# Performance work log

Measured on AMD Instinct MI355X. Metric: run time of the kernel, lower is better.

## Reference

```python
import jax, jax.numpy as jnp
import numpy as np
from jax import lax

B, C, H, W = 2, 256, 128, 128
NC, NP = 80, 9  # num_classes, num_points (3x3 dcn kernel)
PAD = 1


def conv2d(x, w, b=None, pad=1):
    out = lax.conv_general_dilated(x, w, (1, 1), [(pad, pad), (pad, pad)],
                                   dimension_numbers=('NCHW', 'OIHW', 'NCHW'))
    if b is not None:
        out = out + b[None, :, None, None]
    return out


def bilinear_sample(img_bhwc, py, px):
    # zero-padded bilinear sampling; py/px: [B,H,W] float coords
    Hi, Wi = img_bhwc.shape[1], img_bhwc.shape[2]
    y0 = jnp.floor(py)
    x0 = jnp.floor(px)
    wy1 = py - y0
    wx1 = px - x0

    def gather(yc, xc, w):
        valid = (yc >= 0) & (yc <= Hi - 1) & (xc >= 0) & (xc <= Wi - 1)
        yi = jnp.clip(yc, 0, Hi - 1).astype(jnp.int32)
        xi = jnp.clip(xc, 0, Wi - 1).astype(jnp.int32)
        v = jax.vmap(lambda im, yy, xx: im[yy, xx])(img_bhwc, yi, xi)  # [B,H,W,C]
        return v * (w * valid)[..., None]

    return (gather(y0, x0, (1 - wy1) * (1 - wx1)) + gather(y0, x0 + 1, (1 - wy1) * wx1)
            + gather(y0 + 1, x0, wy1 * (1 - wx1)) + gather(y0 + 1, x0 + 1, wy1 * wx1))


def deform_conv(x, offset, weight, mask=None, pad=1):
    # x: [B,C,H,W]; offset: [B,2K,H,W] interleaved (dy,dx) per kernel point;
    # mask: [B,K,H,W] or None (modulated DCN multiplies sampled value by mask as-is)
    kh, kw = weight.shape[2], weight.shape[3]
    xb = jnp.transpose(x, (0, 2, 3, 1))  # [B,H,W,C]
    gy, gx = jnp.meshgrid(jnp.arange(x.shape[2], dtype=x.dtype),
                          jnp.arange(x.shape[3], dtype=x.dtype), indexing='ij')
    acc = 0.
    for k in range(kh * kw):  # fixed structural loop over 9 kernel points
        ky, kx = k // kw, k % kw
        py = gy[None] + (ky - pad) + offset[:, 2 * k]
        px = gx[None] + (kx - pad) + offset[:, 2 * k + 1]
        val = bilinear_sample(xb, py, px)  # [B,H,W,C]
        if mask is not None:
            val = val * mask[:, k][..., None]
        acc = acc + jnp.einsum('bhwc,oc->bohw', val, weight[:, :, ky, kx])
    return acc


def setup_inputs() -> dict:
    key = jax.random.key(0)
    ks = jax.random.split(key, 16)
    d = {"x": jax.random.normal(ks[0], (B, C, H, W), jnp.float32)}

    def w(k, shape):
        return jax.random.normal(k, shape, jnp.float32) * 0.01

    i = 1
    for j in range(3):
        d[f"cls_w{j}"] = w(ks[i], (C, C, 3, 3)); i += 1
        d[f"cls_b{j}"] = jnp.zeros((C,), jnp.float32)
        d[f"reg_w{j}"] = w(ks[i], (C, C, 3, 3)); i += 1
        d[f"reg_b{j}"] = jnp.zeros((C,), jnp.float32)
    d["init_conv_w"] = w(ks[i], (C, C, 3, 3)); i += 1
    d["init_conv_b"] = jnp.zeros((C,), jnp.float32)
    d["init_out_w"] = w(ks[i], (3 * NP, C, 1, 1)); i += 1
    d["init_out_b"] = jnp.zeros((3 * NP,), jnp.float32)
    d["dcn_cls_w"] = w(ks[i], (C, C, 3, 3)); i += 1  # ModulatedDeformConv (bias=False)
    d["cls_out_w"] = w(ks[i], (NC, C, 1, 1)); i += 1
    d["cls_out_b"] = jnp.full((NC,), -4.59511985013459, jnp.float32)  # bias_init_with_prob(0.01)
    d["dcn_ref_w"] = w(ks[i], (C, C, 3, 3)); i += 1  # DeformConv (bias=False)
    d["ref_out_w"] = w(ks[i], (2 * NP, C, 1, 1)); i += 1
    d["ref_out_b"] = jnp.zeros((2 * NP,), jnp.float32)
    return d


def reference(x, cls_w0, cls_b0, reg_w0, reg_b0, cls_w1, cls_b1, reg_w1, reg_b1,
              cls_w2, cls_b2, reg_w2, reg_b2, init_conv_w, init_conv_b,
              init_out_w, init_out_b, dcn_cls_w, cls_out_w, cls_out_b,
              dcn_ref_w, ref_out_w, ref_out_b):
    relu = jax.nn.relu
    cls_feat = x
    for wgt, b in ((cls_w0, cls_b0), (cls_w1, cls_b1), (cls_w2, cls_b2)):
        cls_feat = relu(conv2d(cls_feat, wgt, b, 1))
    pts_feat = x
    for wgt, b in ((reg_w0, reg_b0), (reg_w1, reg_b1), (reg_w2, reg_b2)):
        pts_feat = relu(conv2d(pts_feat, wgt, b, 1))

    pts_out_init = conv2d(relu(conv2d(pts_feat, init_conv_w, init_conv_b, 1)),
                          init_out_w, init_out_b, 0)  # [B,27,H,W]
    o1, o2, mask = (pts_out_init[:, :NP], pts_out_init[:, NP:2 * NP],
                    pts_out_init[:, 2 * NP:])
    offset = jnp.concatenate([o1, o2], axis=1)  # dcn_offset (points_init = 0)

    cls_out = conv2d(relu(deform_conv(cls_feat, offset, dcn_cls_w, mask)),
                     cls_out_w, cls_out_b, 0)
    pts_out_refine = conv2d(relu(deform_conv(pts_feat, offset, dcn_ref_w)),
                            ref_out_w, ref_out_b, 0)
    pts_out_refine = pts_out_refine + lax.stop_gradient(offset)

    # pts2wh_offsets
    pts = pts_out_refine.reshape(B, NP, 2, H, W)
    pts_mean = pts.mean(axis=1, keepdims=True)          # [B,1,2,H,W]
    wh = jnp.abs(pts + pts_mean).max(axis=1)            # [B,2,H,W]
    reg = pts_mean[:, 0]                                # [B,2,H,W]
    return (cls_out, wh, reg)
```

## Files before the change

kernel.cpp:

```cpp
#include <hip/hip_runtime.h>

#define Bn 2
#define Cn 256
#define Hn 128
#define Wn 128
#define HWn 16384
#define NCn 80

typedef __attribute__((ext_vector_type(4))) float f32x4;
typedef __attribute__((ext_vector_type(8))) short bf16x8;

__device__ __forceinline__ float blo(unsigned u) {
    union { unsigned u; float f; } x; x.u = u << 16; return x.f;
}
__device__ __forceinline__ float bhi(unsigned u) {
    union { unsigned u; float f; } x; x.u = u & 0xffff0000u; return x.f;
}
__device__ __forceinline__ unsigned short f2bf(float f) {
    union { float f; unsigned u; } x; x.f = f;
    unsigned u = x.u + 0x7fffu + ((x.u >> 16) & 1u);
    return (unsigned short)(u >> 16);
}

#define GLOAD16(gp, lp) __builtin_amdgcn_global_load_lds( \
    (__attribute__((address_space(1))) unsigned int*)(gp), \
    (__attribute__((address_space(3))) unsigned int*)(lp), 16, 0, 0)

__global__ void zeroK(unsigned short* z) { z[threadIdx.x] = 0; }

__global__ __launch_bounds__(256) void xinK(const float* __restrict__ x,
                                            unsigned short* __restrict__ o) {
    __shared__ float tb[32][33];
    const int b = blockIdx.z;
    const int hw0 = blockIdx.x * 32, c0 = blockIdx.y * 32;
    const int tx = threadIdx.x & 31, ty = threadIdx.x >> 5;
    const float* ip = x + ((size_t)(b * Cn + c0)) * HWn + hw0;
#pragma unroll
    for (int r = 0; r < 4; ++r) tb[ty + 8 * r][tx] = ip[(size_t)(ty + 8 * r) * HWn + tx];
    __syncthreads();
    unsigned short* op = o + ((size_t)(b * HWn + hw0)) * Cn + c0;
#pragma unroll
    for (int r = 0; r < 4; ++r) op[(size_t)(ty + 8 * r) * Cn + tx] = f2bf(tb[tx][ty + 8 * r]);
}

struct WPtrs { const float* p[9]; };
__global__ __launch_bounds__(256) void repackAll(WPtrs wsrc, unsigned short* __restrict__ dst) {
    const int t = blockIdx.x * 256 + threadIdx.x;
    const int widx = t >> 16;
    const int r = t & 65535;
    const float* s = wsrc.p[widx] + (size_t)r * 9;
    float v[9];
#pragma unroll
    for (int k = 0; k < 9; ++k) v[k] = s[k];
    unsigned short* d = dst + (size_t)widx * 589824 + r;
#pragma unroll
    for (int k = 0; k < 9; ++k) d[(size_t)k * 65536] = f2bf(v[k]);
}

struct HPtrs { const float* w[3]; };
__global__ __launch_bounds__(256) void repackHeads(HPtrs hs, unsigned short* __restrict__ dst) {
    const int t = blockIdx.x * 256 + threadIdx.x;
    const int ic = t & 255, row = t >> 8;
    int which, oc, OC;
    if (row < 32)       { which = 0; oc = row;       OC = 27; }
    else if (row < 128) { which = 1; oc = row - 32;  OC = 80; }
    else                { which = 2; oc = row - 128; OC = 18; }
    dst[t] = (oc < OC) ? f2bf(hs.w[which][(size_t)oc * Cn + ic]) : (unsigned short)0;
}

struct CJobs {
    const unsigned short* feat[2];
    const unsigned short* W[2];
    const float* bias[2];
    unsigned short* out[2];
};
__global__ __launch_bounds__(512, 2) void convGemm256(CJobs jobs,
                                                      const unsigned short* __restrict__ zb) {
    const int jz = blockIdx.z;
    const unsigned short* feat = jobs.feat[jz];
    const unsigned short* Wp = jobs.W[jz];
    const float* bias = jobs.bias[jz];
    unsigned short* outp = jobs.out[jz];

    __shared__ __align__(16) unsigned short lA[2][16384];
    __shared__ __align__(16) unsigned short lB[2][16384];
    const int tid = threadIdx.x;
    const int l = tid & 63, w = tid >> 6;
    const int w_oc = w & 1, w_px = w >> 1;
    const int g = (blockIdx.x & 7) * 16 + (blockIdx.x >> 3);
    const int ry0 = g * 2;
    const int b = ry0 >> 7, y0 = ry0 & 127;
    const int lr = l & 15, lg = l >> 4;

    int rI[4], cI[4], dI[4];
#pragma unroll
    for (int i = 0; i < 4; ++i) {
        int ps = (i * 8 + w) * 64 + l;
        rI[i] = ps >> 3;
        cI[i] = ((ps & 7) ^ (rI[i] & 7)) * 8;
        dI[i] = (i * 8 + w) * 512;
    }

    f32x4 acc[8][4];
#pragma unroll
    for (int i = 0; i < 8; ++i)
#pragma unroll
        for (int j = 0; j < 4; ++j) acc[i][j] = (f32x4){0.f, 0.f, 0.f, 0.f};

    auto stage = [&](int p, int bufIdx) {
        const int k = p >> 2, c0 = (p & 3) * 64;
        const int dy = k / 3 - 1, dx = k % 3 - 1;
        const unsigned short* wk = Wp + (size_t)k * 65536 + c0;
        unsigned short* la = lA[bufIdx];
        unsigned short* lb = lB[bufIdx];
#pragma unroll
        for (int i = 0; i < 4; ++i)
            GLOAD16(wk + rI[i] * Cn + cI[i], la + dI[i]);
#pragma unroll
        for (int i = 0; i < 4; ++i) {
            const int s = rI[i];
            const int yy = y0 + (s >> 7) + dy;
            const int xx = (s & 127) + dx;
            const bool v = ((unsigned)yy < (unsigned)Hn) && ((unsigned)xx < (unsigned)Wn);
            const unsigned short* gp = v
                ? feat + (((size_t)(b * Hn + yy)) * Wn + xx) * Cn + c0 + cI[i]
                : zb;
            GLOAD16(gp, lb + dI[i]);
        }
    };

    stage(0, 0);
    __syncthreads();

#pragma unroll 1
    for (int p = 0; p < 36; ++p) {
        const int cur = p & 1;
        if (p < 35) stage(p + 1, cur ^ 1);
        const unsigned short* la = lA[cur];
        const unsigned short* lb = lB[cur];
#pragma unroll
        for (int h = 0; h < 2; ++h) {
            const int ch = h * 4 + lg;
            bf16x8 av[8], bv[4];
#pragma unroll
            for (int fm = 0; fm < 8; ++fm) {
                const int row = w_oc * 128 + fm * 16 + lr;
                av[fm] = *(const bf16x8*)&la[row * 64 + ((ch ^ (row & 7)) * 8)];
            }
#pragma unroll
            for (int fn = 0; fn < 4; ++fn) {
                const int row = w_px * 64 + fn * 16 + lr;
                bv[fn] = *(const bf16x8*)&lb[row * 64 + ((ch ^ (row & 7)) * 8)];
            }
#pragma unroll
            for (int fm = 0; fm < 8; ++fm)
#pragma unroll
                for (int fn = 0; fn < 4; ++fn)
                    acc[fm][fn] = __builtin_amdgcn_mfma_f32_16x16x32_bf16(
                        av[fm], bv[fn], acc[fm][fn], 0, 0, 0);
        }
        __syncthreads();
    }

#pragma unroll
    for (int fm = 0; fm < 8; ++fm) {
        const int oc = w_oc * 128 + fm * 16 + lg * 4;
        const float b0 = bias[oc], b1 = bias[oc + 1], b2 = bias[oc + 2], b3 = bias[oc + 3];
#pragma unroll
        for (int fn = 0; fn < 4; ++fn) {
            const int px = w_px * 64 + fn * 16 + lr;
            f32x4 v = acc[fm][fn];
            unsigned u0 = (unsigned)f2bf(fmaxf(v[0] + b0, 0.f)) | ((unsigned)f2bf(fmaxf(v[1] + b1, 0.f)) << 16);
            unsigned u1 = (unsigned)f2bf(fmaxf(v[2] + b2, 0.f)) | ((unsigned)f2bf(fmaxf(v[3] + b3, 0.f)) << 16);
            uint2 st; st.x = u0; st.y = u1;
            *(uint2*)&outp[(((size_t)(ry0 + (px >> 7))) * Wn + (px & 127)) * Cn + oc] = st;
        }
    }
}

__global__ __launch_bounds__(256, 2) void convGemm(const unsigned short* __restrict__ feat,
                                                   const unsigned short* __restrict__ Wp,
                                                   const float* __restrict__ bias,
                                                   const unsigned short* __restrict__ zb,
                                                   unsigned short* __restrict__ out) {
    __shared__ __align__(16) unsigned short lA[2][8192];
    __shared__ __align__(16) unsigned short lB[2][8192];
    const int tid = threadIdx.x;
    const int l = tid & 63, w = tid >> 6;
    const int w_oc = w & 1, w_px = w >> 1;
    const int ry = (blockIdx.x & 7) * 32 + (blockIdx.x >> 3);
    const int b = ry >> 7, y = ry & 127;
    const int oc0 = blockIdx.y * 128;
    const int lr = l & 15, lg = l >> 4;

    int rI[4], cI[4], dI[4];
#pragma unroll
    for (int i = 0; i < 4; ++i) {
        int ps = (i * 4 + w) * 64 + l;
        rI[i] = ps >> 3;
        cI[i] = ((ps & 7) ^ (rI[i] & 7)) * 8;
        dI[i] = (i * 4 + w) * 512;
    }

    f32x4 acc[4][4];
#pragma unroll
    for (int i = 0; i < 4; ++i)
#pragma unroll
        for (int j = 0; j < 4; ++j) acc[i][j] = (f32x4){0.f, 0.f, 0.f, 0.f};

    auto stage = [&](int p, int bufIdx) {
        const int k = p >> 2, c0 = (p & 3) * 64;
        const int dy = k / 3 - 1, dx = k % 3 - 1;
        const int yy = y + dy;
        const bool vy = (unsigned)yy < (unsigned)Hn;
        const size_t fbase = ((size_t)(b * Hn + yy)) * Wn;
        const unsigned short* wk = Wp + (size_t)k * 65536 + (size_t)oc0 * Cn + c0;
        unsigned short* la = lA[bufIdx];
        unsigned short* lb = lB[bufIdx];
#pragma unroll
        for (int i = 0; i < 4; ++i)
            GLOAD16(wk + rI[i] * Cn + cI[i], la + dI[i]);
#pragma unroll
        for (int i = 0; i < 4; ++i) {
            const int pxs = rI[i] + dx;
            const unsigned short* g = (vy && (unsigned)pxs < (unsigned)Wn)
                ? feat + ((fbase + pxs) * Cn + c0 + cI[i])
                : zb;
            GLOAD16(g, lb + dI[i]);
        }
    };

    stage(0, 0);
    __syncthreads();

#pragma unroll 1
    for (int p = 0; p < 36; ++p) {
        const int cur = p & 1;
        if (p < 35) stage(p + 1, cur ^ 1);
        const unsigned short* la = lA[cur];
        const unsigned short* lb = lB[cur];
#pragma unroll
        for (int h = 0; h < 2; ++h) {
            const int ch = h * 4 + lg;
            bf16x8 av[4], bv[4];
#pragma unroll
            for (int fm = 0; fm < 4; ++fm) {
                const int row = w_oc * 64 + fm * 16 + lr;
                av[fm] = *(const bf16x8*)&la[row * 64 + ((ch ^ (row & 7)) * 8)];
            }
#pragma unroll
            for (int fn = 0; fn < 4; ++fn) {
                const int row = w_px * 64 + fn * 16 + lr;
                bv[fn] = *(const bf16x8*)&lb[row * 64 + ((ch ^ (row & 7)) * 8)];
            }
#pragma unroll
            for (int fm = 0; fm < 4; ++fm)
#pragma unroll
                for (int fn = 0; fn < 4; ++fn)
                    acc[fm][fn] = __builtin_amdgcn_mfma_f32_16x16x32_bf16(
                        av[fm], bv[fn], acc[fm][fn], 0, 0, 0);
        }
        __syncthreads();
    }

#pragma unroll
    for (int fm = 0; fm < 4; ++fm) {
        const int ocb = oc0 + w_oc * 64 + fm * 16 + lg * 4;
        const float b0 = bias[ocb], b1 = bias[ocb + 1], b2 = bias[ocb + 2], b3 = bias[ocb + 3];
#pragma unroll
        for (int fn = 0; fn < 4; ++fn) {
            const int px = w_px * 64 + fn * 16 + lr;
            f32x4 v = acc[fm][fn];
            unsigned u0 = (unsigned)f2bf(fmaxf(v[0] + b0, 0.f)) | ((unsigned)f2bf(fmaxf(v[1] + b1, 0.f)) << 16);
            unsigned u1 = (unsigned)f2bf(fmaxf(v[2] + b2, 0.f)) | ((unsigned)f2bf(fmaxf(v[3] + b3, 0.f)) << 16);
            uint2 st; st.x = u0; st.y = u1;
            *(uint2*)&out[((size_t)ry * Wn + px) * Cn + ocb] = st;
        }
    }
}

struct DJobs {
    const unsigned short* feat[2];
    const unsigned short* W[2];
    unsigned short* out[2];
    int mask[2];
};
__global__ __launch_bounds__(512, 2) void dcnGemm(DJobs jobs,
                                                  const float* __restrict__ o27) {
    const int jz = blockIdx.x >> 8;
    const unsigned short* feat = jobs.feat[jz];
    const unsigned short* Wp = jobs.W[jz];
    unsigned short* outp = jobs.out[jz];
    const bool HASMASK = jobs.mask[jz] != 0;

    __shared__ __align__(16) unsigned short lA[2][16384];
    __shared__ __align__(16) unsigned short lB[2][8192];
    const int tid = threadIdx.x;
    const int l = tid & 63, w = tid >> 6;
    const int w_oc = w & 3, w_px = w >> 2;
    const int lb_ = blockIdx.x & 255;
    const int g = (lb_ & 7) * 32 + (lb_ >> 3);
    const int b = g >> 7, y = g & 127;
    const int lr = l & 15, lg = l >> 4;

    int rIA[4], cIA[4], dIA[4];
#pragma unroll
    for (int i = 0; i < 4; ++i) {
        int ps = (i * 8 + w) * 64 + l;
        rIA[i] = ps >> 3;
        cIA[i] = ((ps & 7) ^ (rIA[i] & 7)) * 8;
        dIA[i] = (i * 8 + w) * 512;
    }

    const int sp = tid >> 2;
    const int pc0 = (tid & 3) * 2;

    const float* ob = o27 + (size_t)b * 27 * HWn + y * Wn + sp;
    const unsigned short* fb = feat + (size_t)b * HWn * Cn;

    f32x4 acc[4][4];
#pragma unroll
    for (int i = 0; i < 4; ++i)
#pragma unroll
        for (int j = 0; j < 4; ++j) acc[i][j] = (f32x4){0.f, 0.f, 0.f, 0.f};

    int ci0, ci1, ci2, ci3;
    float cw0, cw1, cw2, cw3;

    auto sampParams = [&](int k) {
        const float offy = ob[(size_t)(2 * k) * HWn];
        const float offx = ob[(size_t)(2 * k + 1) * HWn];
        const float m = HASMASK ? ob[(size_t)(18 + k) * HWn] : 1.f;
        const float py = (float)(y + k / 3 - 1) + offy;
        const float px = (float)(sp + k % 3 - 1) + offx;
        const float y0f = floorf(py), x0f = floorf(px);
        const float wy1 = py - y0f, wx1 = px - x0f;
        const int iy0 = (int)y0f, ix0 = (int)x0f;
        const int iy1 = iy0 + 1, ix1 = ix0 + 1;
        const bool vy0 = (unsigned)iy0 < (unsigned)Hn, vy1 = (unsigned)iy1 < (unsigned)Hn;
        const bool vx0 = (unsigned)ix0 < (unsigned)Wn, vx1 = (unsigned)ix1 < (unsigned)Wn;
        const int yc0 = min(max(iy0, 0), Hn - 1), yc1 = min(max(iy1, 0), Hn - 1);
        const int xc0 = min(max(ix0, 0), Wn - 1), xc1 = min(max(ix1, 0), Wn - 1);
        cw0 = (vy0 && vx0) ? (1.f - wy1) * (1.f - wx1) * m : 0.f;
        cw1 = (vy0 && vx1) ? (1.f - wy1) * wx1 * m : 0.f;
        cw2 = (vy1 && vx0) ? wy1 * (1.f - wx1) * m : 0.f;
        cw3 = (vy1 && vx1) ? wy1 * wx1 * m : 0.f;
        ci0 = (yc0 * Wn + xc0) * Cn;
        ci1 = (yc0 * Wn + xc1) * Cn;
        ci2 = (yc1 * Wn + xc0) * Cn;
        ci3 = (yc1 * Wn + xc1) * Cn;
    };

    int4 qa0, qa1, qa2, qa3;
    int4 qb0, qb1, qb2, qb3;
    auto cornerLoads = [&](int p) {
        const int cbA = (p & 3) * 64 + pc0 * 8;
        const int cbB = cbA + 8;
        qa0 = *(const int4*)(fb + ci0 + cbA);
        qa1 = *(const int4*)(fb + ci1 + cbA);
        qa2 = *(const int4*)(fb + ci2 + cbA);
        qa3 = *(const int4*)(fb + ci3 + cbA);
        qb0 = *(const int4*)(fb + ci0 + cbB);
        qb1 = *(const int4*)(fb + ci1 + cbB);
        qb2 = *(const int4*)(fb + ci2 + cbB);
        qb3 = *(const int4*)(fb + ci3 + cbB);
    };
    auto stageA = [&](int p, int bufIdx) {
        const int k = p >> 2, c0 = (p & 3) * 64;
        const unsigned short* wk = Wp + (size_t)k * 65536 + c0;
        unsigned short* la = lA[bufIdx];
#pragma unroll
        for (int i = 0; i < 4; ++i)
            GLOAD16(wk + rIA[i] * Cn + cIA[i], la + dIA[i]);
    };
    auto interp1 = [&](int4& c0v, int4& c1v, int4& c2v, int4& c3v) -> int4 {
        unsigned u[4];
#pragma unroll
        for (int jj = 0; jj < 4; ++jj) {
            const unsigned a0 = ((const unsigned*)&c0v)[jj];
            const unsigned a1 = ((const unsigned*)&c1v)[jj];
            const unsigned a2 = ((const unsigned*)&c2v)[jj];
            const unsigned a3 = ((const unsigned*)&c3v)[jj];
            float e0 = cw0 * blo(a0) + cw1 * blo(a1) + cw2 * blo(a2) + cw3 * blo(a3);
            float e1 = cw0 * bhi(a0) + cw1 * bhi(a1) + cw2 * bhi(a2) + cw3 * bhi(a3);
            u[jj] = (unsigned)f2bf(e0) | ((unsigned)f2bf(e1) << 16);
        }
        int4 pk; pk.x = u[0]; pk.y = u[1]; pk.z = u[2]; pk.w = u[3];
        return pk;
    };
    auto interpWrite = [&](int bufIdx) {
        int4 p0 = interp1(qa0, qa1, qa2, qa3);
        int4 p1 = interp1(qb0, qb1, qb2, qb3);
        *(int4*)&lB[bufIdx][sp * 64 + ((pc0 ^ (sp & 7)) * 8)] = p0;
        *(int4*)&lB[bufIdx][sp * 64 + (((pc0 + 1) ^ (sp & 7)) * 8)] = p1;
    };

    sampParams(0);
    stageA(0, 0);
    cornerLoads(0);
    interpWrite(0);
    __syncthreads();

#pragma unroll 1
    for (int p = 0; p < 36; ++p) {
        const int cur = p & 1;
        if (p < 35) {
            if (((p + 1) & 3) == 0) sampParams((p + 1) >> 2);
            stageA(p + 1, cur ^ 1);
            cornerLoads(p + 1);
        }
        const unsigned short* la = lA[cur];
        const unsigned short* lb = lB[cur];
#pragma unroll
        for (int h = 0; h < 2; ++h) {
            const int ch = h * 4 + lg;
            bf16x8 av[4], bv[4];
#pragma unroll
            for (int fm = 0; fm < 4; ++fm) {
                const int row = w_oc * 64 + fm * 16 + lr;
                av[fm] = *(const bf16x8*)&la[row * 64 + ((ch ^ (row & 7)) * 8)];
            }
#pragma unroll
            for (int fn = 0; fn < 4; ++fn) {
                const int row = w_px * 64 + fn * 16 + lr;
                bv[fn] = *(const bf16x8*)&lb[row * 64 + ((ch ^ (row & 7)) * 8)];
            }
#pragma unroll
            for (int fm = 0; fm < 4; ++fm)
#pragma unroll
                for (int fn = 0; fn < 4; ++fn)
                    acc[fm][fn] = __builtin_amdgcn_mfma_f32_16x16x32_bf16(
                        av[fm], bv[fn], acc[fm][fn], 0, 0, 0);
        }
        if (p < 35) interpWrite(cur ^ 1);
        __syncthreads();
    }

#pragma unroll
    for (int fm = 0; fm < 4; ++fm) {
        const int oc = w_oc * 64 + fm * 16 + lg * 4;
#pragma unroll
        for (int fn = 0; fn < 4; ++fn) {
            const int px = w_px * 64 + fn * 16 + lr;
            f32x4 v = acc[fm][fn];
            unsigned u0 = (unsigned)f2bf(fmaxf(v[0], 0.f)) | ((unsigned)f2bf(fmaxf(v[1], 0.f)) << 16);
            unsigned u1 = (unsigned)f2bf(fmaxf(v[2], 0.f)) | ((unsigned)f2bf(fmaxf(v[3], 0.f)) << 16);
            uint2 stv; stv.x = u0; stv.y = u1;
            *(uint2*)&outp[((size_t)g * Wn + px) * Cn + oc] = stv;
        }
    }
}

template <int OC, int PM, bool ADD, bool POST>
__global__ __launch_bounds__(256, 2) void headGemm(const unsigned short* __restrict__ feat,
                                                   const unsigned short* __restrict__ Wp,
                                                   const float* __restrict__ bias,
                                                   float* __restrict__ out,
                                                   const float* __restrict__ add,
                                                   int addC,
                                                   float* __restrict__ reg) {
    constexpr int MF = PM / 16;
    constexpr int NA = PM * 8 / 256;
    __shared__ __align__(16) unsigned short lA[PM * 64];
    __shared__ __align__(16) unsigned short lB[128 * 64];
    __shared__ float lR[POST ? 18 : 1][POST ? 128 : 1];
    const int tid = threadIdx.x;
    const int l = tid & 63, w = tid >> 6;
    const int ry = (blockIdx.x & 7) * 32 + (blockIdx.x >> 3);
    const int b = ry >> 7, y = ry & 127;
    const int lr = l & 15, lg = l >> 4;

    int rIA[NA], cIA[NA], dIA[NA];
#pragma unroll
    for (int i = 0; i < NA; ++i) {
        int ps = (i * 4 + w) * 64 + l;
        rIA[i] = ps >> 3;
        cIA[i] = ((ps & 7) ^ (rIA[i] & 7)) * 8;
        dIA[i] = (i * 4 + w) * 512;
    }
    int rIB[4], cIB[4], dIB[4];
#pragma unroll
    for (int i = 0; i < 4; ++i) {
        int ps = (i * 4 + w) * 64 + l;
        rIB[i] = ps >> 3;
        cIB[i] = ((ps & 7) ^ (rIB[i] & 7)) * 8;
        dIB[i] = (i * 4 + w) * 512;
    }

    f32x4 acc[MF][2];
#pragma unroll
    for (int i = 0; i < MF; ++i)
#pragma unroll
        for (int j = 0; j < 2; ++j) acc[i][j] = (f32x4){0.f, 0.f, 0.f, 0.f};

    const unsigned short* frow = feat + ((size_t)ry * Wn) * Cn;

#pragma unroll 1
    for (int cc = 0; cc < 4; ++cc) {
        const int c0 = cc * 64;
#pragma unroll
        for (int i = 0; i < NA; ++i)
            GLOAD16(Wp + (size_t)rIA[i] * Cn + c0 + cIA[i], &lA[dIA[i]]);
#pragma unroll
        for (int i = 0; i < 4; ++i)
            GLOAD16(frow + (size_t)rIB[i] * Cn + c0 + cIB[i], &lB[dIB[i]]);
        __syncthreads();
#pragma unroll
        for (int h = 0; h < 2; ++h) {
            const int ch = h * 4 + lg;
            bf16x8 av[MF], bv[2];
#pragma unroll
            for (int fm = 0; fm < MF; ++fm) {
                const int row = fm * 16 + lr;
                av[fm] = *(const bf16x8*)&lA[row * 64 + ((ch ^ (row & 7)) * 8)];
            }
#pragma unroll
            for (int fn = 0; fn < 2; ++fn) {
                const int row = w * 32 + fn * 16 + lr;
                bv[fn] = *(const bf16x8*)&lB[row * 64 + ((ch ^ (row & 7)) * 8)];
            }
#pragma unroll
            for (int fm = 0; fm < MF; ++fm)
#pragma unroll
                for (int fn = 0; fn < 2; ++fn)
                    acc[fm][fn] = __builtin_amdgcn_mfma_f32_16x16x32_bf16(
                        av[fm], bv[fn], acc[fm][fn], 0, 0, 0);
        }
        __syncthreads();
    }

    if (!POST) {
#pragma unroll
        for (int fm = 0; fm < MF; ++fm) {
            const int ocb = fm * 16 + lg * 4;
            if (ocb >= OC) break;
#pragma unroll
            for (int j = 0; j < 4; ++j) {
                const int oc = ocb + j;
                if (oc >= OC) break;
                const float bs = bias[oc];
#pragma unroll
                for (int fn = 0; fn < 2; ++fn) {
                    const int px = w * 32 + fn * 16 + lr;
                    float r = acc[fm][fn][j] + bs;
                    if (ADD) r += add[((size_t)(b * addC + oc)) * HWn + y * Wn + px];
                    out[((size_t)(b * OC + oc)) * HWn + y * Wn + px] = r;
                }
            }
        }
    } else {
#pragma unroll
        for (int fm = 0; fm < MF; ++fm) {
            const int ocb = fm * 16 + lg * 4;
#pragma unroll
            for (int j = 0; j < 4; ++j) {
                const int oc = ocb + j;
                if (oc < 18) {
                    const float bs = bias[oc];
#pragma unroll
                    for (int fn = 0; fn < 2; ++fn) {
                        const int px = w * 32 + fn * 16 + lr;
                        float r = acc[fm][fn][j] + bs
                                + add[((size_t)(b * addC + oc)) * HWn + y * Wn + px];
                        lR[oc][px] = r;
                    }
                }
            }
        }
        __syncthreads();
        if (tid < 128) {
            const int px = tid;
            float v[18];
#pragma unroll
            for (int c = 0; c < 18; ++c) v[c] = lR[c][px];
            float s0 = 0.f, s1 = 0.f;
#pragma unroll
            for (int q = 0; q < 9; ++q) { s0 += v[2 * q]; s1 += v[2 * q + 1]; }
            float m0 = s0 * (1.f / 9.f), m1 = s1 * (1.f / 9.f);
            float w0 = 0.f, w1 = 0.f;
#pragma unroll
            for (int q = 0; q < 9; ++q) {
                w0 = fmaxf(w0, fabsf(v[2 * q] + m0));
                w1 = fmaxf(w1, fabsf(v[2 * q + 1] + m1));
            }
            const size_t hw = (size_t)y * Wn + px;
            out[(size_t)(b * 2 + 0) * HWn + hw] = w0;
            out[(size_t)(b * 2 + 1) * HWn + hw] = w1;
            reg[(size_t)(b * 2 + 0) * HWn + hw] = m0;
            reg[(size_t)(b * 2 + 1) * HWn + hw] = m1;
        }
    }
}

extern "C" void kernel_launch(void* const* d_in, const int* in_sizes, int n_in,
                              void* d_out, int out_size, void* d_ws, size_t ws_size,
                              hipStream_t stream) {
    const float* x           = (const float*)d_in[0];
    const float* cls_w0      = (const float*)d_in[1];
    const float* cls_b0      = (const float*)d_in[2];
    const float* reg_w0      = (const float*)d_in[3];
    const float* reg_b0      = (const float*)d_in[4];
    const float* cls_w1      = (const float*)d_in[5];
    const float* cls_b1      = (const float*)d_in[6];
    const float* reg_w1      = (const float*)d_in[7];
    const float* reg_b1      = (const float*)d_in[8];
    const float* cls_w2      = (const float*)d_in[9];
    const float* cls_b2      = (const float*)d_in[10];
    const float* reg_w2      = (const float*)d_in[11];
    const float* reg_b2      = (const float*)d_in[12];
    const float* init_conv_w = (const float*)d_in[13];
    const float* init_conv_b = (const float*)d_in[14];
    const float* init_out_w  = (const float*)d_in[15];
    const float* init_out_b  = (const float*)d_in[16];
    const float* dcn_cls_w   = (const float*)d_in[17];
    const float* cls_out_w   = (const float*)d_in[18];
    const float* cls_out_b   = (const float*)d_in[19];
    const float* dcn_ref_w   = (const float*)d_in[20];
    const float* ref_out_w   = (const float*)d_in[21];
    const float* ref_out_b   = (const float*)d_in[22];

    float* out = (float*)d_out;

    char* ws = (char*)d_ws;
    const size_t IMG = (size_t)Bn * HWn * Cn * sizeof(unsigned short);
    unsigned short* B0 = (unsigned short*)ws; ws += IMG;
    unsigned short* B1 = (unsigned short*)ws; ws += IMG;
    unsigned short* B2 = (unsigned short*)ws; ws += IMG;
    unsigned short* B3 = (unsigned short*)ws; ws += IMG;
    float* O27 = (float*)ws; ws += (size_t)Bn * 27 * HWn * sizeof(float);
    const size_t WSZ = (size_t)9 * Cn * Cn;
    unsigned short* Wpk = (unsigned short*)ws; ws += 9 * WSZ * sizeof(unsigned short);
    unsigned short* WhAll = (unsigned short*)ws; ws += 160 * Cn * sizeof(unsigned short);
    unsigned short* ZB = (unsigned short*)ws;  ws += 512;

    unsigned short* W_cls0 = Wpk + 0 * WSZ;
    unsigned short* W_cls1 = Wpk + 1 * WSZ;
    unsigned short* W_cls2 = Wpk + 2 * WSZ;
    unsigned short* W_reg0 = Wpk + 3 * WSZ;
    unsigned short* W_reg1 = Wpk + 4 * WSZ;
    unsigned short* W_reg2 = Wpk + 5 * WSZ;
    unsigned short* W_init = Wpk + 6 * WSZ;
    unsigned short* W_dcls = Wpk + 7 * WSZ;
    unsigned short* W_dref = Wpk + 8 * WSZ;
    unsigned short* Wh27 = WhAll;
    unsigned short* Wh80 = WhAll + 32 * Cn;
    unsigned short* Wh18 = WhAll + 128 * Cn;

    const dim3 blk(256);
    const dim3 blk5(512);
    const dim3 xgrd(512, 8, Bn);

    zeroK<<<1, 128, 0, stream>>>(ZB);
    WPtrs wp;
    wp.p[0] = cls_w0; wp.p[1] = cls_w1; wp.p[2] = cls_w2;
    wp.p[3] = reg_w0; wp.p[4] = reg_w1; wp.p[5] = reg_w2;
    wp.p[6] = init_conv_w; wp.p[7] = dcn_cls_w; wp.p[8] = dcn_ref_w;
    repackAll<<<2304, blk, 0, stream>>>(wp, Wpk);
    HPtrs hp; hp.w[0] = init_out_w; hp.w[1] = cls_out_w; hp.w[2] = ref_out_w;
    repackHeads<<<160, blk, 0, stream>>>(hp, WhAll);
    xinK<<<xgrd, blk, 0, stream>>>(x, B0);

    CJobs j;
    j.feat[0] = B0; j.W[0] = W_cls0; j.bias[0] = cls_b0; j.out[0] = B1;
    j.feat[1] = B0; j.W[1] = W_reg0; j.bias[1] = reg_b0; j.out[1] = B2;
    convGemm256<<<dim3(128, 1, 2), blk5, 0, stream>>>(j, ZB);
    j.feat[0] = B1; j.W[0] = W_cls1; j.bias[0] = cls_b1; j.out[0] = B3;
    j.feat[1] = B2; j.W[1] = W_reg1; j.bias[1] = reg_b1; j.out[1] = B0;
    convGemm256<<<dim3(128, 1, 2), blk5, 0, stream>>>(j, ZB);
    j.feat[0] = B3; j.W[0] = W_cls2; j.bias[0] = cls_b2; j.out[0] = B1;
    j.feat[1] = B0; j.W[1] = W_reg2; j.bias[1] = reg_b2; j.out[1] = B2;
    convGemm256<<<dim3(128, 1, 2), blk5, 0, stream>>>(j, ZB);
    convGemm<<<dim3(256, 2, 1), blk, 0, stream>>>(B2, W_init, init_conv_b, ZB, B3);
    headGemm<27, 32, false, false><<<256, blk, 0, stream>>>(B3, Wh27, init_out_b, O27, nullptr, 0, nullptr);
    DJobs dj;
    dj.feat[0] = B1; dj.W[0] = W_dcls; dj.out[0] = B0; dj.mask[0] = 1;
    dj.feat[1] = B2; dj.W[1] = W_dref; dj.out[1] = B3; dj.mask[1] = 0;
    dcnGemm<<<512, blk5, 0, stream>>>(dj, O27);
    headGemm<80, 96, false, false><<<256, blk, 0, stream>>>(B0, Wh80, cls_out_b, out, nullptr, 0, nullptr);
    headGemm<18, 32, true, true><<<256, blk, 0, stream>>>(
        B3, Wh18, ref_out_b,
        out + (size_t)Bn * NCn * HWn,
        O27, 27,
        out + (size_t)Bn * NCn * HWn + (size_t)Bn * 2 * HWn);
}
```

Baseline: 594.1 us.

## Halve DCN pixel tile, deepen gather pipeline, use packed bf16 convert

The deformable-conv GEMM now processes half a row (64 pixels) per block, doubling the grid and targeting 4 blocks per CU with a smaller B tile. The bilinear gather is re-pipelined: each thread handles one 8-channel chunk, corner loads are issued two stages ahead, and offset loads and sample parameters for the next kernel point are computed while MFMAs run. Bf16 packing across all GEMM epilogues switches to the hardware v_cvt_pk_bf16_f32 instruction, and the zero-buffer kernel is folded into the repack kernel. The smaller tiles reduce weight reuse per block and add register pressure in exchange for more latency hiding of the irregular gathers.

Result: slower. 689.6 us (+16.1%).

```diff
diff --git a/kernel.cpp b/kernel.cpp
--- a/kernel.cpp
+++ b/kernel.cpp
@@ -13,20 +13,23 @@
 __device__ __forceinline__ float blo(unsigned u) {
     union { unsigned u; float f; } x; x.u = u << 16; return x.f;
 }
-__device__ __forceinline__ float bhi(unsigned u) {
-    union { unsigned u; float f; } x; x.u = u & 0xffff0000u; return x.f;
+__device__ __forceinline__ float braw(unsigned u) {
+    union { unsigned u; float f; } x; x.u = u; return x.f;
 }
 __device__ __forceinline__ unsigned short f2bf(float f) {
     union { float f; unsigned u; } x; x.f = f;
     unsigned u = x.u + 0x7fffu + ((x.u >> 16) & 1u);
     return (unsigned short)(u >> 16);
 }
+__device__ __forceinline__ unsigned pk2bf(float e0, float e1) {
+    unsigned r;
+    asm("v_cvt_pk_bf16_f32 %0, %1, %2" : "=v"(r) : "v"(e0), "v"(e1));
+    return r;
+}
 
 #define GLOAD16(gp, lp) __builtin_amdgcn_global_load_lds( \
     (__attribute__((address_space(1))) unsigned int*)(gp), \
     (__attribute__((address_space(3))) unsigned int*)(lp), 16, 0, 0)
-
-__global__ void zeroK(unsigned short* z) { z[threadIdx.x] = 0; }
 
 __global__ __launch_bounds__(256) void xinK(const float* __restrict__ x,
                                             unsigned short* __restrict__ o) {
@@ -44,7 +47,9 @@
 }
 
 struct WPtrs { const float* p[9]; };
-__global__ __launch_bounds__(256) void repackAll(WPtrs wsrc, unsigned short* __restrict__ dst) {
+__global__ __launch_bounds__(256) void repackAll(WPtrs wsrc, unsigned short* __restrict__ dst,
+                                                 unsigned short* __restrict__ zb) {
+    if (blockIdx.x == 0) { zb[threadIdx.x] = 0; zb[256 + threadIdx.x] = 0; }
     const int t = blockIdx.x * 256 + threadIdx.x;
     const int widx = t >> 16;
     const int r = t & 65535;
@@ -74,6 +79,7 @@
     const float* bias[2];
     unsigned short* out[2];
 };
+
 __global__ __launch_bounds__(512, 2) void convGemm256(CJobs jobs,
                                                       const unsigned short* __restrict__ zb) {
     const int jz = blockIdx.z;
@@ -170,9 +176,9 @@
         for (int fn = 0; fn < 4; ++fn) {
             const int px = w_px * 64 + fn * 16 + lr;
             f32x4 v = acc[fm][fn];
-            unsigned u0 = (unsigned)f2bf(fmaxf(v[0] + b0, 0.f)) | ((unsigned)f2bf(fmaxf(v[1] + b1, 0.f)) << 16);
-            unsigned u1 = (unsigned)f2bf(fmaxf(v[2] + b2, 0.f)) | ((unsigned)f2bf(fmaxf(v[3] + b3, 0.f)) << 16);
-            uint2 st; st.x = u0; st.y = u1;
+            uint2 st;
+            st.x = pk2bf(fmaxf(v[0] + b0, 0.f), fmaxf(v[1] + b1, 0.f));
+            st.y = pk2bf(fmaxf(v[2] + b2, 0.f), fmaxf(v[3] + b3, 0.f));
             *(uint2*)&outp[(((size_t)(ry0 + (px >> 7))) * Wn + (px & 127)) * Cn + oc] = st;
         }
     }
@@ -271,9 +277,9 @@
         for (int fn = 0; fn < 4; ++fn) {
             const int px = w_px * 64 + fn * 16 + lr;
             f32x4 v = acc[fm][fn];
-            unsigned u0 = (unsigned)f2bf(fmaxf(v[0] + b0, 0.f)) | ((unsigned)f2bf(fmaxf(v[1] + b1, 0.f)) << 16);
-            unsigned u1 = (unsigned)f2bf(fmaxf(v[2] + b2, 0.f)) | ((unsigned)f2bf(fmaxf(v[3] + b3, 0.f)) << 16);
-            uint2 st; st.x = u0; st.y = u1;
+            uint2 st;
+            st.x = pk2bf(fmaxf(v[0] + b0, 0.f), fmaxf(v[1] + b1, 0.f));
+            st.y = pk2bf(fmaxf(v[2] + b2, 0.f), fmaxf(v[3] + b3, 0.f));
             *(uint2*)&out[((size_t)ry * Wn + px) * Cn + ocb] = st;
         }
     }
@@ -285,22 +291,24 @@
     unsigned short* out[2];
     int mask[2];
 };
-__global__ __launch_bounds__(512, 2) void dcnGemm(DJobs jobs,
+__global__ __launch_bounds__(512, 4) void dcnGemm(DJobs jobs,
                                                   const float* __restrict__ o27) {
-    const int jz = blockIdx.x >> 8;
+    const int jz = blockIdx.x >> 9;
     const unsigned short* feat = jobs.feat[jz];
     const unsigned short* Wp = jobs.W[jz];
     unsigned short* outp = jobs.out[jz];
     const bool HASMASK = jobs.mask[jz] != 0;
 
     __shared__ __align__(16) unsigned short lA[2][16384];
-    __shared__ __align__(16) unsigned short lB[2][8192];
+    __shared__ __align__(16) unsigned short lB[2][4096];
     const int tid = threadIdx.x;
     const int l = tid & 63, w = tid >> 6;
     const int w_oc = w & 3, w_px = w >> 2;
-    const int lb_ = blockIdx.x & 255;
-    const int g = (lb_ & 7) * 32 + (lb_ >> 3);
-    const int b = g >> 7, y = g & 127;
+    const int lb_ = blockIdx.x & 511;
+    const int g = (lb_ & 7) * 64 + (lb_ >> 3);
+    const int ry = g >> 1, st = g & 1;
+    const int b = ry >> 7, y = ry & 127;
+    const int x0 = st * 64;
     const int lr = l & 15, lg = l >> 4;
 
     int rIA[4], cIA[4], dIA[4];
@@ -312,27 +320,29 @@
         dIA[i] = (i * 8 + w) * 512;
     }
 
-    const int sp = tid >> 2;
-    const int pc0 = (tid & 3) * 2;
-
-    const float* ob = o27 + (size_t)b * 27 * HWn + y * Wn + sp;
+    const int sp = tid >> 3;
+    const int pc = tid & 7;
+    const int xg = x0 + sp;
+    const int wslot = sp * 64 + ((pc ^ (sp & 7)) * 8);
+
+    const float* ob = o27 + (size_t)b * 27 * HWn + y * Wn + xg;
     const unsigned short* fb = feat + (size_t)b * HWn * Cn;
 
-    f32x4 acc[4][4];
+    f32x4 acc[4][2];
 #pragma unroll
     for (int i = 0; i < 4; ++i)
 #pragma unroll
-        for (int j = 0; j < 4; ++j) acc[i][j] = (f32x4){0.f, 0.f, 0.f, 0.f};
-
-    int ci0, ci1, ci2, ci3;
-    float cw0, cw1, cw2, cw3;
-
-    auto sampParams = [&](int k) {
-        const float offy = ob[(size_t)(2 * k) * HWn];
-        const float offx = ob[(size_t)(2 * k + 1) * HWn];
-        const float m = HASMASK ? ob[(size_t)(18 + k) * HWn] : 1.f;
+        for (int j = 0; j < 2; ++j) acc[i][j] = (f32x4){0.f, 0.f, 0.f, 0.f};
+
+    int ci0, ci1, ci2, ci3;        float cw0, cw1, cw2, cw3;
+    int ni0, ni1, ni2, ni3;        float nw0, nw1, nw2, nw3;
+    float pofy, pofx, pom;
+
+    auto sampCompute = [&](int k, float offy, float offx, float m,
+                           int& o0, int& o1, int& o2, int& o3,
+                           float& u0, float& u1, float& u2, float& u3) {
         const float py = (float)(y + k / 3 - 1) + offy;
-        const float px = (float)(sp + k % 3 - 1) + offx;
+        const float px = (float)(xg + k % 3 - 1) + offx;
         const float y0f = floorf(py), x0f = floorf(px);
         const float wy1 = py - y0f, wx1 = px - x0f;
         const int iy0 = (int)y0f, ix0 = (int)x0f;
@@ -341,98 +351,118 @@
         const bool vx0 = (unsigned)ix0 < (unsigned)Wn, vx1 = (unsigned)ix1 < (unsigned)Wn;
         const int yc0 = min(max(iy0, 0), Hn - 1), yc1 = min(max(iy1, 0), Hn - 1);
         const int xc0 = min(max(ix0, 0), Wn - 1), xc1 = min(max(ix1, 0), Wn - 1);
-        cw0 = (vy0 && vx0) ? (1.f - wy1) * (1.f - wx1) * m : 0.f;
-        cw1 = (vy0 && vx1) ? (1.f - wy1) * wx1 * m : 0.f;
-        cw2 = (vy1 && vx0) ? wy1 * (1.f - wx1) * m : 0.f;
-        cw3 = (vy1 && vx1) ? wy1 * wx1 * m : 0.f;
-        ci0 = (yc0 * Wn + xc0) * Cn;
-        ci1 = (yc0 * Wn + xc1) * Cn;
-        ci2 = (yc1 * Wn + xc0) * Cn;
-        ci3 = (yc1 * Wn + xc1) * Cn;
+        u0 = (vy0 && vx0) ? (1.f - wy1) * (1.f - wx1) * m : 0.f;
+        u1 = (vy0 && vx1) ? (1.f - wy1) * wx1 * m : 0.f;
+        u2 = (vy1 && vx0) ? wy1 * (1.f - wx1) * m : 0.f;
+        u3 = (vy1 && vx1) ? wy1 * wx1 * m : 0.f;
+        o0 = (yc0 * Wn + xc0) * Cn;
+        o1 = (yc0 * Wn + xc1) * Cn;
+        o2 = (yc1 * Wn + xc0) * Cn;
+        o3 = (yc1 * Wn + xc1) * Cn;
     };
 
     int4 qa0, qa1, qa2, qa3;
     int4 qb0, qb1, qb2, qb3;
-    auto cornerLoads = [&](int p) {
-        const int cbA = (p & 3) * 64 + pc0 * 8;
-        const int cbB = cbA + 8;
-        qa0 = *(const int4*)(fb + ci0 + cbA);
-        qa1 = *(const int4*)(fb + ci1 + cbA);
-        qa2 = *(const int4*)(fb + ci2 + cbA);
-        qa3 = *(const int4*)(fb + ci3 + cbA);
-        qb0 = *(const int4*)(fb + ci0 + cbB);
-        qb1 = *(const int4*)(fb + ci1 + cbB);
-        qb2 = *(const int4*)(fb + ci2 + cbB);
-        qb3 = *(const int4*)(fb + ci3 + cbB);
-    };
-    auto stageA = [&](int p, int bufIdx) {
-        const int k = p >> 2, c0 = (p & 3) * 64;
+
+#define DFILL(Q0, Q1, Q2, Q3, I0, I1, I2, I3, CBI) do { \
+        const int cb_ = (CBI) * 64 + pc * 8; \
+        Q0 = *(const int4*)(fb + (I0) + cb_); \
+        Q1 = *(const int4*)(fb + (I1) + cb_); \
+        Q2 = *(const int4*)(fb + (I2) + cb_); \
+        Q3 = *(const int4*)(fb + (I3) + cb_); \
+    } while (0)
+
+#define DWRITE(Q0, Q1, Q2, Q3, U0, U1, U2, U3, BUF) do { \
+        unsigned uu[4]; \
+        _Pragma("unroll") for (int jj = 0; jj < 4; ++jj) { \
+            const unsigned a0 = ((const unsigned*)&Q0)[jj]; \
+            const unsigned a1 = ((const unsigned*)&Q1)[jj]; \
+            const unsigned a2 = ((const unsigned*)&Q2)[jj]; \
+            const unsigned a3 = ((const unsigned*)&Q3)[jj]; \
+            float e0 = U0 * blo(a0) + U1 * blo(a1) + U2 * blo(a2) + U3 * blo(a3); \
+            float e1 = U0 * braw(a0) + U1 * braw(a1) + U2 * braw(a2) + U3 * braw(a3); \
+            uu[jj] = pk2bf(e0, e1); \
+        } \
+        int4 pk_; pk_.x = uu[0]; pk_.y = uu[1]; pk_.z = uu[2]; pk_.w = uu[3]; \
+        *(int4*)&lB[BUF][wslot] = pk_; \
+    } while (0)
+
+    auto stageA = [&](int p) {
+        const int k = p >> 2, c0 = (p & 3) * 64, bf = p & 1;
         const unsigned short* wk = Wp + (size_t)k * 65536 + c0;
-        unsigned short* la = lA[bufIdx];
+        unsigned short* la = lA[bf];
 #pragma unroll
         for (int i = 0; i < 4; ++i)
             GLOAD16(wk + rIA[i] * Cn + cIA[i], la + dIA[i]);
     };
-    auto interp1 = [&](int4& c0v, int4& c1v, int4& c2v, int4& c3v) -> int4 {
-        unsigned u[4];
-#pragma unroll
-        for (int jj = 0; jj < 4; ++jj) {
-            const unsigned a0 = ((const unsigned*)&c0v)[jj];
-            const unsigned a1 = ((const unsigned*)&c1v)[jj];
-            const unsigned a2 = ((const unsigned*)&c2v)[jj];
-            const unsigned a3 = ((const unsigned*)&c3v)[jj];
-            float e0 = cw0 * blo(a0) + cw1 * blo(a1) + cw2 * blo(a2) + cw3 * blo(a3);
-            float e1 = cw0 * bhi(a0) + cw1 * bhi(a1) + cw2 * bhi(a2) + cw3 * bhi(a3);
-            u[jj] = (unsigned)f2bf(e0) | ((unsigned)f2bf(e1) << 16);
-        }
-        int4 pk; pk.x = u[0]; pk.y = u[1]; pk.z = u[2]; pk.w = u[3];
-        return pk;
-    };
-    auto interpWrite = [&](int bufIdx) {
-        int4 p0 = interp1(qa0, qa1, qa2, qa3);
-        int4 p1 = interp1(qb0, qb1, qb2, qb3);
-        *(int4*)&lB[bufIdx][sp * 64 + ((pc0 ^ (sp & 7)) * 8)] = p0;
-        *(int4*)&lB[bufIdx][sp * 64 + (((pc0 + 1) ^ (sp & 7)) * 8)] = p1;
-    };
-
-    sampParams(0);
-    stageA(0, 0);
-    cornerLoads(0);
-    interpWrite(0);
+
+#define DMFMA(BUF) do { \
+        const unsigned short* la_ = lA[BUF]; \
+        const unsigned short* lb2_ = lB[BUF]; \
+        _Pragma("unroll") for (int h = 0; h < 2; ++h) { \
+            const int ch = h * 4 + lg; \
+            bf16x8 av[4], bv[2]; \
+            _Pragma("unroll") for (int fm = 0; fm < 4; ++fm) { \
+                const int row = w_oc * 64 + fm * 16 + lr; \
+                av[fm] = *(const bf16x8*)&la_[row * 64 + ((ch ^ (row & 7)) * 8)]; } \
+            _Pragma("unroll") for (int fn = 0; fn < 2; ++fn) { \
+                const int row = w_px * 32 + fn * 16 + lr; \
+                bv[fn] = *(const bf16x8*)&lb2_[row * 64 + ((ch ^ (row & 7)) * 8)]; } \
+            _Pragma("unroll") for (int fm = 0; fm < 4; ++fm) \
+                _Pragma("unroll") for (int fn = 0; fn < 2; ++fn) \
+                    acc[fm][fn] = __builtin_amdgcn_mfma_f32_16x16x32_bf16( \
+                        av[fm], bv[fn], acc[fm][fn], 0, 0, 0); \
+        } \
+    } while (0)
+
+    {
+        const float offy = ob[0];
+        const float offx = ob[(size_t)HWn];
+        const float m = HASMASK ? ob[(size_t)18 * HWn] : 1.f;
+        sampCompute(0, offy, offx, m, ci0, ci1, ci2, ci3, cw0, cw1, cw2, cw3);
+    }
+    DFILL(qa0, qa1, qa2, qa3, ci0, ci1, ci2, ci3, 0);
+    stageA(0);
+    DWRITE(qa0, qa1, qa2, qa3, cw0, cw1, cw2, cw3, 0);
+    DFILL(qb0, qb1, qb2, qb3, ci0, ci1, ci2, ci3, 1);
     __syncthreads();
 
 #pragma unroll 1
-    for (int p = 0; p < 36; ++p) {
-        const int cur = p & 1;
-        if (p < 35) {
-            if (((p + 1) & 3) == 0) sampParams((p + 1) >> 2);
-            stageA(p + 1, cur ^ 1);
-            cornerLoads(p + 1);
-        }
-        const unsigned short* la = lA[cur];
-        const unsigned short* lb = lB[cur];
-#pragma unroll
-        for (int h = 0; h < 2; ++h) {
-            const int ch = h * 4 + lg;
-            bf16x8 av[4], bv[4];
-#pragma unroll
-            for (int fm = 0; fm < 4; ++fm) {
-                const int row = w_oc * 64 + fm * 16 + lr;
-                av[fm] = *(const bf16x8*)&la[row * 64 + ((ch ^ (row & 7)) * 8)];
-            }
-#pragma unroll
-            for (int fn = 0; fn < 4; ++fn) {
-                const int row = w_px * 64 + fn * 16 + lr;
-                bv[fn] = *(const bf16x8*)&lb[row * 64 + ((ch ^ (row & 7)) * 8)];
-            }
-#pragma unroll
-            for (int fm = 0; fm < 4; ++fm)
-#pragma unroll
-                for (int fn = 0; fn < 4; ++fn)
-                    acc[fm][fn] = __builtin_amdgcn_mfma_f32_16x16x32_bf16(
-                        av[fm], bv[fn], acc[fm][fn], 0, 0, 0);
-        }
-        if (p < 35) interpWrite(cur ^ 1);
+    for (int kk = 0; kk < 9; ++kk) {
+        const bool moreK = (kk < 8);
+        if (moreK) {
+            const int kn = kk + 1;
+            pofy = ob[(size_t)(2 * kn) * HWn];
+            pofx = ob[(size_t)(2 * kn + 1) * HWn];
+            pom = HASMASK ? ob[(size_t)(18 + kn) * HWn] : 1.f;
+        }
+        stageA(4 * kk + 1);
+        DFILL(qa0, qa1, qa2, qa3, ci0, ci1, ci2, ci3, 2);
+        DMFMA(0);
+        DWRITE(qb0, qb1, qb2, qb3, cw0, cw1, cw2, cw3, 1);
+        __syncthreads();
+        if (moreK)
+            sampCompute(kk + 1, pofy, pofx, pom, ni0, ni1, ni2, ni3, nw0, nw1, nw2, nw3);
+        stageA(4 * kk + 2);
+        DFILL(qb0, qb1, qb2, qb3, ci0, ci1, ci2, ci3, 3);
+        DMFMA(1);
+        DWRITE(qa0, qa1, qa2, qa3, cw0, cw1, cw2, cw3, 0);
+        __syncthreads();
+        stageA(4 * kk + 3);
+        if (moreK) DFILL(qa0, qa1, qa2, qa3, ni0, ni1, ni2, ni3, 0);
+        DMFMA(0);
+        DWRITE(qb0, qb1, qb2, qb3, cw0, cw1, cw2, cw3, 1);
+        __syncthreads();
+        if (moreK) {
+            stageA(4 * kk + 4);
+            DFILL(qb0, qb1, qb2, qb3, ni0, ni1, ni2, ni3, 1);
+        }
+        DMFMA(1);
+        if (moreK) {
+            DWRITE(qa0, qa1, qa2, qa3, nw0, nw1, nw2, nw3, 0);
+            ci0 = ni0; ci1 = ni1; ci2 = ni2; ci3 = ni3;
+            cw0 = nw0; cw1 = nw1; cw2 = nw2; cw3 = nw3;
+        }
         __syncthreads();
     }
 
@@ -440,15 +470,18 @@
     for (int fm = 0; fm < 4; ++fm) {
         const int oc = w_oc * 64 + fm * 16 + lg * 4;
 #pragma unroll
-        for (int fn = 0; fn < 4; ++fn) {
-            const int px = w_px * 64 + fn * 16 + lr;
+        for (int fn = 0; fn < 2; ++fn) {
+            const int px = x0 + w_px * 32 + fn * 16 + lr;
             f32x4 v = acc[fm][fn];
-            unsigned u0 = (unsigned)f2bf(fmaxf(v[0], 0.f)) | ((unsigned)f2bf(fmaxf(v[1], 0.f)) << 16);
-            unsigned u1 = (unsigned)f2bf(fmaxf(v[2], 0.f)) | ((unsigned)f2bf(fmaxf(v[3], 0.f)) << 16);
-            uint2 stv; stv.x = u0; stv.y = u1;
-            *(uint2*)&outp[((size_t)g * Wn + px) * Cn + oc] = stv;
-        }
-    }
+            uint2 stv;
+            stv.x = pk2bf(fmaxf(v[0], 0.f), fmaxf(v[1], 0.f));
+            stv.y = pk2bf(fmaxf(v[2], 0.f), fmaxf(v[3], 0.f));
+            *(uint2*)&outp[((size_t)ry * Wn + px) * Cn + oc] = stv;
+        }
+    }
+#undef DFILL
+#undef DWRITE
+#undef DMFMA
 }
 
 template <int OC, int PM, bool ADD, bool POST>
@@ -631,7 +664,7 @@
     const size_t WSZ = (size_t)9 * Cn * Cn;
     unsigned short* Wpk = (unsigned short*)ws; ws += 9 * WSZ * sizeof(unsigned short);
     unsigned short* WhAll = (unsigned short*)ws; ws += 160 * Cn * sizeof(unsigned short);
-    unsigned short* ZB = (unsigned short*)ws;  ws += 512;
+    unsigned short* ZB = (unsigned short*)ws;  ws += 1024;
 
     unsigned short* W_cls0 = Wpk + 0 * WSZ;
     unsigned short* W_cls1 = Wpk + 1 * WSZ;
@@ -650,12 +683,11 @@
     const dim3 blk5(512);
     const dim3 xgrd(512, 8, Bn);
 
-    zeroK<<<1, 128, 0, stream>>>(ZB);
     WPtrs wp;
     wp.p[0] = cls_w0; wp.p[1] = cls_w1; wp.p[2] = cls_w2;
     wp.p[3] = reg_w0; wp.p[4] = reg_w1; wp.p[5] = reg_w2;
     wp.p[6] = init_conv_w; wp.p[7] = dcn_cls_w; wp.p[8] = dcn_ref_w;
-    repackAll<<<2304, blk, 0, stream>>>(wp, Wpk);
+    repackAll<<<2304, blk, 0, stream>>>(wp, Wpk, ZB);
     HPtrs hp; hp.w[0] = init_out_w; hp.w[1] = cls_out_w; hp.w[2] = ref_out_w;
     repackHeads<<<160, blk, 0, stream>>>(hp, WhAll);
     xinK<<<xgrd, blk, 0, stream>>>(x, B0);
@@ -675,7 +707,7 @@
     DJobs dj;
     dj.feat[0] = B1; dj.W[0] = W_dcls; dj.out[0] = B0; dj.mask[0] = 1;
     dj.feat[1] = B2; dj.W[1] = W_dref; dj.out[1] = B3; dj.mask[1] = 0;
-    dcnGemm<<<512, blk5, 0, stream>>>(dj, O27);
+    dcnGemm<<<1024, blk5, 0, stream>>>(dj, O27);
     headGemm<80, 96, false, false><<<256, blk, 0, stream>>>(B0, Wh80, cls_out_b, out, nullptr, 0, nullptr);
     headGemm<18, 32, true, true><<<256, blk, 0, stream>>>(
         B3, Wh18, ref_out_b,
```
